# Kernel optimization log

Hardware: AMD Instinct MI355X
Metric: run time of the kernel (lower is better)

Reference implementation:

```python
import jax, jax.numpy as jnp
import numpy as np

N = 100000
E = 1600000
IN_DIM = 128
OUT_DIM = 128
H = 4
HD = OUT_DIM // H  # 32
NEG_SLOPE = 0.2
EPS_SOFTMAX = 1e-8
EPS_LN = 1e-5


def setup_inputs() -> dict:
    key = jax.random.key(0)
    ks = jax.random.split(key, 6)
    h = jax.random.normal(ks[0], (N, IN_DIM), dtype=jnp.float32)
    edge_index = jax.random.randint(ks[1], (2, E), 0, N, dtype=jnp.int32)
    W = jax.random.normal(ks[2], (IN_DIM, OUT_DIM), dtype=jnp.float32) / np.sqrt(IN_DIM)
    W_self = jax.random.normal(ks[3], (IN_DIM, OUT_DIM), dtype=jnp.float32) / np.sqrt(IN_DIM)
    a_in = jax.random.normal(ks[4], (H, 2 * HD), dtype=jnp.float32) * 0.01
    a_out = jax.random.normal(ks[5], (H, 2 * HD), dtype=jnp.float32) * 0.01
    bias = jnp.zeros((OUT_DIM,), dtype=jnp.float32)
    ln_gamma = jnp.ones((OUT_DIM,), dtype=jnp.float32)
    ln_beta = jnp.zeros((OUT_DIM,), dtype=jnp.float32)
    return {"h": h, "edge_index": edge_index, "W": W, "W_self": W_self,
            "a_in": a_in, "a_out": a_out, "bias": bias,
            "ln_gamma": ln_gamma, "ln_beta": ln_beta}


def _attention_aggregate(h_proj, sender, receiver, attn_vec, num_nodes):
    # h_proj: (N, H, HD); sender/receiver: (E,); attn_vec: (H, 2*HD)
    h_sender = h_proj[sender]      # (E, H, HD)
    h_receiver = h_proj[receiver]  # (E, H, HD)
    # e = sum over concat([h_sender, h_receiver]) * attn_vec, split halves
    e = (jnp.einsum('ehd,hd->eh', h_sender, attn_vec[:, :HD])
         + jnp.einsum('ehd,hd->eh', h_receiver, attn_vec[:, HD:]))
    e = jax.nn.leaky_relu(e, NEG_SLOPE)
    e_max = jax.ops.segment_max(e, receiver, num_segments=num_nodes)  # (N, H)
    alpha = jnp.exp(e - e_max[receiver])
    alpha_sum = jax.ops.segment_sum(alpha, receiver, num_segments=num_nodes)
    alpha = alpha / (alpha_sum[receiver] + EPS_SOFTMAX)
    msg = h_sender * alpha[..., None]  # (E, H, HD)
    return jax.ops.segment_sum(msg, receiver, num_segments=num_nodes)  # (N, H, HD)


def reference(h, edge_index, W, W_self, a_in, a_out, bias, ln_gamma, ln_beta):
    n = h.shape[0]
    h_proj = (h @ W).reshape(n, H, HD)
    h_self = h @ W_self
    src, dst = edge_index[0], edge_index[1]
    h_in = _attention_aggregate(h_proj, src, dst, a_in, n)   # 'in' direction
    h_out = _attention_aggregate(h_proj, dst, src, a_out, n)  # 'out' direction
    combined = h_self + h_in.reshape(n, -1) + h_out.reshape(n, -1) + bias
    mean = combined.mean(axis=-1, keepdims=True)
    var = combined.var(axis=-1, keepdims=True)
    normed = (combined - mean) * jax.lax.rsqrt(var + EPS_LN)
    return normed * ln_gamma + ln_beta
```

## Files before the change

kernel.cpp:

```cpp
#include <hip/hip_runtime.h>
#include <math.h>

#define HEADS 4
#define HD 32
#define DIM 128
#define NEG_SLOPE 0.2f
#define EPS_SM 1e-8f
#define EPS_LN 1e-5f
#define GROWS 64
#define SH1 9
#define PB 128

__device__ __forceinline__ float lrelu(float x) { return x > 0.f ? x : NEG_SLOPE * x; }
__device__ __forceinline__ unsigned bf16rne(float x) {
    unsigned b = __float_as_uint(x);
    return (b + 0x7fffu + ((b >> 16) & 1u)) >> 16;
}

template<int LIM> __device__ __forceinline__ void rmax4(float& a, float& b, float& c, float& d) {
#pragma unroll
    for (int s = 1; s < LIM; s <<= 1) {
        a = fmaxf(a, __shfl_xor(a, s, 64));
        b = fmaxf(b, __shfl_xor(b, s, 64));
        c = fmaxf(c, __shfl_xor(c, s, 64));
        d = fmaxf(d, __shfl_xor(d, s, 64));
    }
}
template<int LIM> __device__ __forceinline__ void rsum4(float& a, float& b, float& c, float& d) {
#pragma unroll
    for (int s = 1; s < LIM; s <<= 1) {
        a += __shfl_xor(a, s, 64);
        b += __shfl_xor(b, s, 64);
        c += __shfl_xor(c, s, 64);
        d += __shfl_xor(d, s, 64);
    }
}

__global__ __launch_bounds__(256) void dual_gemm_k(const float* __restrict__ h,
                                                   const float* __restrict__ W,
                                                   const float* __restrict__ V,
                                                   const float* __restrict__ a_in,
                                                   const float* __restrict__ a_out,
                                                   float* __restrict__ h_self,
                                                   unsigned* __restrict__ hp_pk,
                                                   float* __restrict__ pA0, float* __restrict__ pA1,
                                                   float* __restrict__ pB0, float* __restrict__ pB1,
                                                   int N) {
    __shared__ float As[32][GROWS];
    __shared__ float Ws[32][DIM];
    __shared__ float Vs[32][DIM];
    __shared__ float ainL[256], aoutL[256];
    const int tid = threadIdx.x;
    const int cg = tid & 15;
    const int rg = tid >> 4;
    const int row0 = blockIdx.x * GROWS;

    ainL[tid] = a_in[tid];
    aoutL[tid] = a_out[tid];

    float accP[4][8], accS[4][8];
#pragma unroll
    for (int r = 0; r < 4; ++r)
#pragma unroll
        for (int c = 0; c < 8; ++c) { accP[r][c] = 0.f; accS[r][c] = 0.f; }

    for (int kc = 0; kc < 4; ++kc) {
        __syncthreads();
#pragma unroll
        for (int p = 0; p < 2; ++p) {
            int f = tid + p * 256;
            int r = f >> 3, c4 = f & 7;
            float4 v = make_float4(0.f, 0.f, 0.f, 0.f);
            if (row0 + r < N) v = ((const float4*)h)[(size_t)(row0 + r) * 32 + kc * 8 + c4];
            As[c4 * 4 + 0][r] = v.x;
            As[c4 * 4 + 1][r] = v.y;
            As[c4 * 4 + 2][r] = v.z;
            As[c4 * 4 + 3][r] = v.w;
        }
#pragma unroll
        for (int p = 0; p < 4; ++p) {
            int f = tid + p * 256;
            int lk = f >> 5, c4 = f & 31;
            ((float4*)&Ws[lk][0])[c4] = ((const float4*)W)[(size_t)(kc * 32 + lk) * 32 + c4];
            ((float4*)&Vs[lk][0])[c4] = ((const float4*)V)[(size_t)(kc * 32 + lk) * 32 + c4];
        }
        __syncthreads();
#pragma unroll
        for (int kk = 0; kk < 32; ++kk) {
            float4 a = *(const float4*)&As[kk][rg * 4];
            float4 w0 = *(const float4*)&Ws[kk][cg * 8];
            float4 w1 = *(const float4*)&Ws[kk][cg * 8 + 4];
            float4 v0 = *(const float4*)&Vs[kk][cg * 8];
            float4 v1 = *(const float4*)&Vs[kk][cg * 8 + 4];
            float av[4] = {a.x, a.y, a.z, a.w};
            float wv[8] = {w0.x, w0.y, w0.z, w0.w, w1.x, w1.y, w1.z, w1.w};
            float vv[8] = {v0.x, v0.y, v0.z, v0.w, v1.x, v1.y, v1.z, v1.w};
#pragma unroll
            for (int r = 0; r < 4; ++r)
#pragma unroll
                for (int c = 0; c < 8; ++c) {
                    accP[r][c] += av[r] * wv[c];
                    accS[r][c] += av[r] * vv[c];
                }
        }
    }

#pragma unroll
    for (int r = 0; r < 4; ++r) {
        int row = row0 + rg * 4 + r;
        if (row < N) {
            float4 s0 = make_float4(accS[r][0], accS[r][1], accS[r][2], accS[r][3]);
            float4 s1 = make_float4(accS[r][4], accS[r][5], accS[r][6], accS[r][7]);
            ((float4*)h_self)[(size_t)row * 32 + cg * 2] = s0;
            ((float4*)h_self)[(size_t)row * 32 + cg * 2 + 1] = s1;
        }
    }

    const int head = cg >> 2, qi = cg & 3;
#pragma unroll
    for (int r = 0; r < 4; ++r) {
        float d0 = 0.f, d1 = 0.f, d2 = 0.f, d3 = 0.f;
#pragma unroll
        for (int c = 0; c < 8; ++c) {
            float v = accP[r][c];
            int k = head * 64 + qi * 8 + c;
            d0 += v * ainL[k];
            d1 += v * ainL[k + 32];
            d2 += v * aoutL[k];
            d3 += v * aoutL[k + 32];
        }
        d0 += __shfl_xor(d0, 1, 64); d0 += __shfl_xor(d0, 2, 64);
        d1 += __shfl_xor(d1, 1, 64); d1 += __shfl_xor(d1, 2, 64);
        d2 += __shfl_xor(d2, 1, 64); d2 += __shfl_xor(d2, 2, 64);
        d3 += __shfl_xor(d3, 1, 64); d3 += __shfl_xor(d3, 2, 64);
        if (qi == 0) {
            int row = row0 + rg * 4 + r;
            if (row < N) {
                pA0[row * 4 + head] = d0;
                pA1[row * 4 + head] = d1;
                pB0[row * 4 + head] = d2;
                pB1[row * 4 + head] = d3;
            }
        }
    }

    __syncthreads();
    float* lds2 = &Ws[0][0];
    if (cg >= 8) {
#pragma unroll
        for (int r = 0; r < 4; ++r) {
            int rl = rg * 4 + r;
#pragma unroll
            for (int c = 0; c < 8; ++c) lds2[rl * 64 + (cg - 8) * 8 + c] = accP[r][c];
        }
    }
    __syncthreads();
    if (cg < 8) {
#pragma unroll
        for (int r = 0; r < 4; ++r) {
            int rl = rg * 4 + r;
            int row = row0 + rl;
            if (row < N) {
                unsigned pks[8];
#pragma unroll
                for (int c = 0; c < 8; ++c)
                    pks[c] = bf16rne(accP[r][c]) | (bf16rne(lds2[rl * 64 + cg * 8 + c]) << 16);
                uint4* dst = (uint4*)(hp_pk + (size_t)row * 64 + cg * 8);
                dst[0] = make_uint4(pks[0], pks[1], pks[2], pks[3]);
                dst[1] = make_uint4(pks[4], pks[5], pks[6], pks[7]);
            }
        }
    }
}

__global__ __launch_bounds__(256) void part1a_k(const int* __restrict__ ei, int* __restrict__ cntmat,
                                                int E, int N, int NBIN) {
    __shared__ int lcnt[512];
    const int t = threadIdx.x;
    const int CH = (E + gridDim.x - 1) / gridDim.x;
    const int e0 = blockIdx.x * CH;
    const int e1 = min(e0 + CH, E);
    for (int i = t; i < 512; i += 256) lcnt[i] = 0;
    __syncthreads();
    for (int e = e0 + t; e < e1; e += 256) {
        int s = ei[e], d = ei[E + e];
        atomicAdd(&lcnt[d >> SH1], 1);
        atomicAdd(&lcnt[(N + s) >> SH1], 1);
    }
    __syncthreads();
    for (int i = t; i < NBIN; i += 256) cntmat[i * PB + blockIdx.x] = lcnt[i];
}

__global__ __launch_bounds__(128) void scanB_k(const int* __restrict__ cntmat,
                                               int* __restrict__ blkoff, int* __restrict__ btot) {
    __shared__ int ls[PB];
    const int bin = blockIdx.x;
    const int t = threadIdx.x;
    int v = cntmat[bin * PB + t];
    ls[t] = v;
    __syncthreads();
#pragma unroll
    for (int d = 1; d < PB; d <<= 1) {
        int u = (t >= d) ? ls[t - d] : 0;
        __syncthreads();
        ls[t] += u;
        __syncthreads();
    }
    blkoff[bin * PB + t] = ls[t] - v;
    if (t == PB - 1) btot[bin] = ls[t];
}

__global__ __launch_bounds__(256) void scanC_k(const int* __restrict__ btot,
                                               int* __restrict__ bbase, int NBIN, int twoE) {
    __shared__ int ls[256];
    int t = threadIdx.x;
    int i0 = 2 * t, i1 = 2 * t + 1;
    int v0 = (i0 < NBIN) ? btot[i0] : 0;
    int v1 = (i1 < NBIN) ? btot[i1] : 0;
    int pair = v0 + v1;
    ls[t] = pair;
    __syncthreads();
#pragma unroll
    for (int d = 1; d < 256; d <<= 1) {
        int u = (t >= d) ? ls[t - d] : 0;
        __syncthreads();
        ls[t] += u;
        __syncthreads();
    }
    int excl = ls[t] - pair;
    if (i0 < NBIN) bbase[i0] = excl;
    if (i1 < NBIN) bbase[i1] = excl + v0;
    if (t == 0) bbase[NBIN] = twoE;
}

__global__ __launch_bounds__(256) void part1b_k(const int* __restrict__ ei,
                                                const int* __restrict__ bbase,
                                                const int* __restrict__ blkoff,
                                                unsigned* __restrict__ rec, int E, int N, int NBIN) {
    __shared__ int gb[512];
    __shared__ int lcur[512];
    const int t = threadIdx.x;
    const int CH = (E + gridDim.x - 1) / gridDim.x;
    const int e0 = blockIdx.x * CH;
    const int e1 = min(e0 + CH, E);
    for (int i = t; i < 512; i += 256) lcur[i] = 0;
    for (int i = t; i < NBIN; i += 256) gb[i] = bbase[i] + blkoff[i * PB + blockIdx.x];
    __syncthreads();
    for (int e = e0 + t; e < e1; e += 256) {
        int s = ei[e], d = ei[E + e];
        int b1 = d >> SH1;
        int r1 = atomicAdd(&lcur[b1], 1);
        rec[gb[b1] + r1] = (unsigned)s | ((unsigned)(d & 511) << 20);
        int so = N + s;
        int b2 = so >> SH1;
        int r2 = atomicAdd(&lcur[b2], 1);
        rec[gb[b2] + r2] = (unsigned)d | ((unsigned)(so & 511) << 20);
    }
}

__global__ __launch_bounds__(256) void build2_k(const unsigned* __restrict__ rec,
                                                const int* __restrict__ bbase,
                                                int* __restrict__ off, int* __restrict__ csr,
                                                int M, int twoE, int NBIN) {
    __shared__ int lcnt[512];
    __shared__ int lcur[512];
    __shared__ int ls[256];
    const int b = blockIdx.x;
    const int t = threadIdx.x;
    const int base = bbase[b];
    const int cnt = bbase[b + 1] - base;
    const int seg0 = b << SH1;
    for (int i = t; i < 512; i += 256) lcnt[i] = 0;
    __syncthreads();
    for (int k = t; k < cnt; k += 256) atomicAdd(&lcnt[rec[base + k] >> 20], 1);
    __syncthreads();
    int v0 = lcnt[2 * t], v1 = lcnt[2 * t + 1];
    int pair = v0 + v1;
    ls[t] = pair;
    __syncthreads();
#pragma unroll
    for (int d = 1; d < 256; d <<= 1) {
        int u = (t >= d) ? ls[t - d] : 0;
        __syncthreads();
        ls[t] += u;
        __syncthreads();
    }
    int excl = ls[t] - pair;
    lcur[2 * t] = excl;
    lcur[2 * t + 1] = excl + v0;
    int sg = seg0 + 2 * t;
    if (sg < M) off[sg] = base + excl;
    if (sg + 1 < M) off[sg + 1] = base + excl + v0;
    if (b == NBIN - 1 && t == 0) off[M] = twoE;
    __syncthreads();
    for (int k = t; k < cnt; k += 256) {
        unsigned r = rec[base + k];
        int pos = atomicAdd(&lcur[r >> 20], 1);
        csr[base + pos] = (int)(r & 0xFFFFFu);
    }
}

__global__ __launch_bounds__(256) void node_aggr_ln_k(const unsigned* __restrict__ hp_pk,
                                                      const float* __restrict__ h_self,
                                                      const float* __restrict__ pA0, const float* __restrict__ pA1,
                                                      const float* __restrict__ pB0, const float* __restrict__ pB1,
                                                      const int* __restrict__ off, const int* __restrict__ csr,
                                                      const float* __restrict__ bias,
                                                      const float* __restrict__ gamma,
                                                      const float* __restrict__ beta,
                                                      float* __restrict__ out, int N) {
    __shared__ uint4 lw[4][64];
    const int wave = threadIdx.x >> 6;
    const int lane = threadIdx.x & 63;
    const int n = blockIdx.x * 4 + wave;
    if (n >= N) return;
    const int l15 = lane & 15;
    const int q = lane >> 4;
    const unsigned lwoff = (unsigned)((q << 4) + ((l15 >> 3) << 3));
    const char* lwbase = (const char*)&lw[wave][0];
    const uint4* __restrict__ hpp4 = (const uint4*)hp_pk;

    float alo0 = 0.f, alo1 = 0.f, alo2 = 0.f, alo3 = 0.f;
    float ahi0 = 0.f, ahi1 = 0.f, ahi2 = 0.f, ahi3 = 0.f;

#pragma unroll
    for (int dir = 0; dir < 2; ++dir) {
        const int seg = (dir == 0) ? n : N + n;
        const int beg = off[seg], end = off[seg + 1];
        const int len = end - beg;
        if (len == 0) continue;
        const float* __restrict__ p0 = (dir == 0) ? pA0 : pB0;
        const float* __restrict__ p1 = (dir == 0) ? pA1 : pB1;
        float4 r1 = ((const float4*)p1)[n];

        if (len <= 64) {
            int sid = 0;
            float e0 = -INFINITY, e1 = -INFINITY, e2 = -INFINITY, e3 = -INFINITY;
            if (lane < len) {
                sid = csr[beg + lane];
                float4 r0 = ((const float4*)p0)[sid];
                e0 = lrelu(r0.x + r1.x);
                e1 = lrelu(r0.y + r1.y);
                e2 = lrelu(r0.z + r1.z);
                e3 = lrelu(r0.w + r1.w);
            }
            float m0 = e0, m1 = e1, m2 = e2, m3 = e3;
            if (len <= 16)      rmax4<16>(m0, m1, m2, m3);
            else if (len <= 32) rmax4<32>(m0, m1, m2, m3);
            else                rmax4<64>(m0, m1, m2, m3);
            float w0 = 0.f, w1 = 0.f, w2 = 0.f, w3 = 0.f;
            if (lane < len) {
                w0 = expf(e0 - m0); w1 = expf(e1 - m1);
                w2 = expf(e2 - m2); w3 = expf(e3 - m3);
            }
            float s0 = w0, s1 = w1, s2 = w2, s3 = w3;
            if (len <= 16)      rsum4<16>(s0, s1, s2, s3);
            else if (len <= 32) rsum4<32>(s0, s1, s2, s3);
            else                rsum4<64>(s0, s1, s2, s3);
            w0 *= 1.f / (s0 + EPS_SM);
            w1 *= 1.f / (s1 + EPS_SM);
            w2 *= 1.f / (s2 + EPS_SM);
            w3 *= 1.f / (s3 + EPS_SM);
            unsigned pkA = bf16rne(w0) | (bf16rne(w2) << 16);
            unsigned pkB = bf16rne(w1) | (bf16rne(w3) << 16);
            lw[wave][lane] = make_uint4(pkA, (unsigned)sid, pkB, (unsigned)sid);
            const int nt = (len + 3) >> 2;
#pragma unroll 2
            for (int t = 0; t < nt; ++t) {
                uint2 wv = *(const uint2*)(lwbase + t * 64 + lwoff);
                uint4 v = hpp4[((size_t)wv.y << 4) + l15];
                float wa = __uint_as_float(wv.x << 16);
                float wb = __uint_as_float(wv.x & 0xffff0000u);
                alo0 += wa * __uint_as_float(v.x << 16);
                ahi0 += wb * __uint_as_float(v.x & 0xffff0000u);
                alo1 += wa * __uint_as_float(v.y << 16);
                ahi1 += wb * __uint_as_float(v.y & 0xffff0000u);
                alo2 += wa * __uint_as_float(v.z << 16);
                ahi2 += wb * __uint_as_float(v.z & 0xffff0000u);
                alo3 += wa * __uint_as_float(v.w << 16);
                ahi3 += wb * __uint_as_float(v.w & 0xffff0000u);
            }
        } else {
            float m0 = -INFINITY, m1 = -INFINITY, m2 = -INFINITY, m3 = -INFINITY;
            for (int base = beg; base < end; base += 64) {
                int j = base + lane;
                if (j < end) {
                    int sid = csr[j];
                    float4 r0 = ((const float4*)p0)[sid];
                    m0 = fmaxf(m0, lrelu(r0.x + r1.x));
                    m1 = fmaxf(m1, lrelu(r0.y + r1.y));
                    m2 = fmaxf(m2, lrelu(r0.z + r1.z));
                    m3 = fmaxf(m3, lrelu(r0.w + r1.w));
                }
            }
            rmax4<64>(m0, m1, m2, m3);
            float s0 = 0.f, s1 = 0.f, s2 = 0.f, s3 = 0.f;
            for (int base = beg; base < end; base += 64) {
                int j = base + lane;
                if (j < end) {
                    int sid = csr[j];
                    float4 r0 = ((const float4*)p0)[sid];
                    s0 += expf(lrelu(r0.x + r1.x) - m0);
                    s1 += expf(lrelu(r0.y + r1.y) - m1);
                    s2 += expf(lrelu(r0.z + r1.z) - m2);
                    s3 += expf(lrelu(r0.w + r1.w) - m3);
                }
            }
            rsum4<64>(s0, s1, s2, s3);
            const float is0 = 1.f / (s0 + EPS_SM);
            const float is1 = 1.f / (s1 + EPS_SM);
            const float is2 = 1.f / (s2 + EPS_SM);
            const float is3 = 1.f / (s3 + EPS_SM);
            for (int base = beg; base < end; base += 64) {
                int cnt = min(64, end - base);
                int sid = 0;
                float w0 = 0.f, w1 = 0.f, w2 = 0.f, w3 = 0.f;
                if (lane < cnt) {
                    sid = csr[base + lane];
                    float4 r0 = ((const float4*)p0)[sid];
                    w0 = expf(lrelu(r0.x + r1.x) - m0) * is0;
                    w1 = expf(lrelu(r0.y + r1.y) - m1) * is1;
                    w2 = expf(lrelu(r0.z + r1.z) - m2) * is2;
                    w3 = expf(lrelu(r0.w + r1.w) - m3) * is3;
                }
                unsigned pkA = bf16rne(w0) | (bf16rne(w2) << 16);
                unsigned pkB = bf16rne(w1) | (bf16rne(w3) << 16);
                lw[wave][lane] = make_uint4(pkA, (unsigned)sid, pkB, (unsigned)sid);
                const int nt = (cnt + 3) >> 2;
#pragma unroll 2
                for (int t = 0; t < nt; ++t) {
                    uint2 wv = *(const uint2*)(lwbase + t * 64 + lwoff);
                    uint4 v = hpp4[((size_t)wv.y << 4) + l15];
                    float wa = __uint_as_float(wv.x << 16);
                    float wb = __uint_as_float(wv.x & 0xffff0000u);
                    alo0 += wa * __uint_as_float(v.x << 16);
                    ahi0 += wb * __uint_as_float(v.x & 0xffff0000u);
                    alo1 += wa * __uint_as_float(v.y << 16);
                    ahi1 += wb * __uint_as_float(v.y & 0xffff0000u);
                    alo2 += wa * __uint_as_float(v.z << 16);
                    ahi2 += wb * __uint_as_float(v.z & 0xffff0000u);
                    alo3 += wa * __uint_as_float(v.w << 16);
                    ahi3 += wb * __uint_as_float(v.w & 0xffff0000u);
                }
            }
        }
    }

#pragma unroll
    for (int s = 16; s < 64; s <<= 1) {
        alo0 += __shfl_xor(alo0, s, 64); alo1 += __shfl_xor(alo1, s, 64);
        alo2 += __shfl_xor(alo2, s, 64); alo3 += __shfl_xor(alo3, s, 64);
        ahi0 += __shfl_xor(ahi0, s, 64); ahi1 += __shfl_xor(ahi1, s, 64);
        ahi2 += __shfl_xor(ahi2, s, 64); ahi3 += __shfl_xor(ahi3, s, 64);
    }

    size_t bb = (size_t)n * DIM;
    float4 hs0 = *(const float4*)(h_self + bb + 4 * l15);
    float4 hs1 = *(const float4*)(h_self + bb + 64 + 4 * l15);
    float4 b0 = *(const float4*)(bias + 4 * l15);
    float4 b1 = *(const float4*)(bias + 64 + 4 * l15);
    float x0 = hs0.x + alo0 + b0.x;
    float x1 = hs0.y + alo1 + b0.y;
    float x2 = hs0.z + alo2 + b0.z;
    float x3 = hs0.w + alo3 + b0.w;
    float y0 = hs1.x + ahi0 + b1.x;
    float y1 = hs1.y + ahi1 + b1.y;
    float y2 = hs1.z + ahi2 + b1.z;
    float y3 = hs1.w + ahi3 + b1.w;
    float sum = x0 + x1 + x2 + x3 + y0 + y1 + y2 + y3;
    float sq = x0 * x0 + x1 * x1 + x2 * x2 + x3 * x3
             + y0 * y0 + y1 * y1 + y2 * y2 + y3 * y3;
#pragma unroll
    for (int m = 1; m < 64; m <<= 1) {
        sum += __shfl_xor(sum, m, 64);
        sq += __shfl_xor(sq, m, 64);
    }
    float mean = sum * (1.f / 512.f);
    float var = sq * (1.f / 512.f) - mean * mean;
    float inv = rsqrtf(var + EPS_LN);
    if (lane < 16) {
        float4 g0 = *(const float4*)(gamma + 4 * l15);
        float4 g1 = *(const float4*)(gamma + 64 + 4 * l15);
        float4 be0 = *(const float4*)(beta + 4 * l15);
        float4 be1 = *(const float4*)(beta + 64 + 4 * l15);
        float4 o0 = make_float4((x0 - mean) * inv * g0.x + be0.x,
                                (x1 - mean) * inv * g0.y + be0.y,
                                (x2 - mean) * inv * g0.z + be0.z,
                                (x3 - mean) * inv * g0.w + be0.w);
        float4 o1 = make_float4((y0 - mean) * inv * g1.x + be1.x,
                                (y1 - mean) * inv * g1.y + be1.y,
                                (y2 - mean) * inv * g1.z + be1.z,
                                (y3 - mean) * inv * g1.w + be1.w);
        *(float4*)(out + bb + 4 * l15) = o0;
        *(float4*)(out + bb + 64 + 4 * l15) = o1;
    }
}

extern "C" void kernel_launch(void* const* d_in, const int* in_sizes, int n_in,
                              void* d_out, int out_size, void* d_ws, size_t ws_size,
                              hipStream_t stream) {
    const float* h      = (const float*)d_in[0];
    const int*   ei     = (const int*)d_in[1];
    const float* W      = (const float*)d_in[2];
    const float* W_self = (const float*)d_in[3];
    const float* a_in   = (const float*)d_in[4];
    const float* a_out  = (const float*)d_in[5];
    const float* bias   = (const float*)d_in[6];
    const float* gamma  = (const float*)d_in[7];
    const float* beta   = (const float*)d_in[8];
    float* out = (float*)d_out;

    const int N = in_sizes[0] / DIM;
    const int E = in_sizes[1] / 2;
    const int M = 2 * N;
    const int NBIN = (M + (1 << SH1) - 1) >> SH1;
    const int twoE = 2 * E;

    float* ws = (float*)d_ws;
    size_t off_f = 0;
    float* h_self = ws + off_f; off_f += (size_t)N * DIM;
    unsigned* hp_pk = (unsigned*)(ws + off_f); off_f += (size_t)N * 64;
    float* pA0 = ws + off_f; off_f += (size_t)N * 4;
    float* pA1 = ws + off_f; off_f += (size_t)N * 4;
    float* pB0 = ws + off_f; off_f += (size_t)N * 4;
    float* pB1 = ws + off_f; off_f += (size_t)N * 4;
    int* ip = (int*)(ws + off_f);
    size_t off_i = 0;
    int* cntmat = ip + off_i; off_i += (size_t)NBIN * PB;
    int* blkoff = ip + off_i; off_i += (size_t)NBIN * PB;
    int* btot   = ip + off_i; off_i += NBIN;
    int* bbase  = ip + off_i; off_i += (size_t)NBIN + 1;
    int* off    = ip + off_i; off_i += (size_t)M + 1;
    unsigned* rec = (unsigned*)(ip + off_i); off_i += (size_t)twoE;
    int* csr    = ip + off_i; off_i += (size_t)twoE;

    part1a_k<<<PB, 256, 0, stream>>>(ei, cntmat, E, N, NBIN);
    scanB_k<<<NBIN, PB, 0, stream>>>(cntmat, blkoff, btot);
    scanC_k<<<1, 256, 0, stream>>>(btot, bbase, NBIN, twoE);
    part1b_k<<<PB, 256, 0, stream>>>(ei, bbase, blkoff, rec, E, N, NBIN);
    build2_k<<<NBIN, 256, 0, stream>>>(rec, bbase, off, csr, M, twoE, NBIN);

    dual_gemm_k<<<(N + GROWS - 1) / GROWS, 256, 0, stream>>>(h, W, W_self, a_in, a_out,
                                                             h_self, hp_pk, pA0, pA1, pB0, pB1, N);

    node_aggr_ln_k<<<(N + 3) / 4, 256, 0, stream>>>(hp_pk, h_self, pA0, pA1, pB0, pB1,
                                                    off, csr, bias, gamma, beta, out, N);
}
```

Measured before the change: 454.3 us.

## Drop softmax max pass, use fast exp, packed FMA, and prefetch GEMM tiles

Removes the segment-max computation from the edge softmax and exponentiates logits directly with __expf, eliminating a full gather pass for long segments and the max shuffles for short ones. The accumulation is restructured as float2 FMAs to encourage packed FMA instructions. The dual GEMM now prefetches the next K chunk into registers while computing the current one. Skipping max-subtraction risks overflow if logits were large, and it adds register pressure in the GEMM.

```diff
diff --git a/kernel.cpp b/kernel.cpp
--- a/kernel.cpp
+++ b/kernel.cpp
@@ -16,16 +16,10 @@
     unsigned b = __float_as_uint(x);
     return (b + 0x7fffu + ((b >> 16) & 1u)) >> 16;
 }
-
-template<int LIM> __device__ __forceinline__ void rmax4(float& a, float& b, float& c, float& d) {
-#pragma unroll
-    for (int s = 1; s < LIM; s <<= 1) {
-        a = fmaxf(a, __shfl_xor(a, s, 64));
-        b = fmaxf(b, __shfl_xor(b, s, 64));
-        c = fmaxf(c, __shfl_xor(c, s, 64));
-        d = fmaxf(d, __shfl_xor(d, s, 64));
-    }
-}
+__device__ __forceinline__ float2 pkfma(float2 v, float2 w, float2 c) {
+    return make_float2(fmaf(v.x, w.x, c.x), fmaf(v.y, w.y, c.y));
+}
+
 template<int LIM> __device__ __forceinline__ void rsum4(float& a, float& b, float& c, float& d) {
 #pragma unroll
     for (int s = 1; s < LIM; s <<= 1) {
@@ -64,27 +58,45 @@
 #pragma unroll
         for (int c = 0; c < 8; ++c) { accP[r][c] = 0.f; accS[r][c] = 0.f; }
 
-    for (int kc = 0; kc < 4; ++kc) {
-        __syncthreads();
+    float4 pha[2], pw[4], pv[4];
+    auto load_chunk = [&](int kc) {
 #pragma unroll
         for (int p = 0; p < 2; ++p) {
             int f = tid + p * 256;
             int r = f >> 3, c4 = f & 7;
             float4 v = make_float4(0.f, 0.f, 0.f, 0.f);
             if (row0 + r < N) v = ((const float4*)h)[(size_t)(row0 + r) * 32 + kc * 8 + c4];
-            As[c4 * 4 + 0][r] = v.x;
-            As[c4 * 4 + 1][r] = v.y;
-            As[c4 * 4 + 2][r] = v.z;
-            As[c4 * 4 + 3][r] = v.w;
+            pha[p] = v;
         }
 #pragma unroll
         for (int p = 0; p < 4; ++p) {
             int f = tid + p * 256;
             int lk = f >> 5, c4 = f & 31;
-            ((float4*)&Ws[lk][0])[c4] = ((const float4*)W)[(size_t)(kc * 32 + lk) * 32 + c4];
-            ((float4*)&Vs[lk][0])[c4] = ((const float4*)V)[(size_t)(kc * 32 + lk) * 32 + c4];
-        }
-        __syncthreads();
+            pw[p] = ((const float4*)W)[(size_t)(kc * 32 + lk) * 32 + c4];
+            pv[p] = ((const float4*)V)[(size_t)(kc * 32 + lk) * 32 + c4];
+        }
+    };
+
+    load_chunk(0);
+    for (int kc = 0; kc < 4; ++kc) {
+#pragma unroll
+        for (int p = 0; p < 2; ++p) {
+            int f = tid + p * 256;
+            int r = f >> 3, c4 = f & 7;
+            As[c4 * 4 + 0][r] = pha[p].x;
+            As[c4 * 4 + 1][r] = pha[p].y;
+            As[c4 * 4 + 2][r] = pha[p].z;
+            As[c4 * 4 + 3][r] = pha[p].w;
+        }
+#pragma unroll
+        for (int p = 0; p < 4; ++p) {
+            int f = tid + p * 256;
+            int lk = f >> 5, c4 = f & 31;
+            ((float4*)&Ws[lk][0])[c4] = pw[p];
+            ((float4*)&Vs[lk][0])[c4] = pv[p];
+        }
+        __syncthreads();
+        if (kc < 3) load_chunk(kc + 1);
 #pragma unroll
         for (int kk = 0; kk < 32; ++kk) {
             float4 a = *(const float4*)&As[kk][rg * 4];
@@ -103,6 +115,7 @@
                     accS[r][c] += av[r] * vv[c];
                 }
         }
+        __syncthreads();
     }
 
 #pragma unroll
@@ -320,8 +333,8 @@
     const char* lwbase = (const char*)&lw[wave][0];
     const uint4* __restrict__ hpp4 = (const uint4*)hp_pk;
 
-    float alo0 = 0.f, alo1 = 0.f, alo2 = 0.f, alo3 = 0.f;
-    float ahi0 = 0.f, ahi1 = 0.f, ahi2 = 0.f, ahi3 = 0.f;
+    float2 a0 = make_float2(0.f, 0.f), a1 = make_float2(0.f, 0.f);
+    float2 a2 = make_float2(0.f, 0.f), a3 = make_float2(0.f, 0.f);
 
 #pragma unroll
     for (int dir = 0; dir < 2; ++dir) {
@@ -335,23 +348,14 @@
 
         if (len <= 64) {
             int sid = 0;
-            float e0 = -INFINITY, e1 = -INFINITY, e2 = -INFINITY, e3 = -INFINITY;
+            float w0 = 0.f, w1 = 0.f, w2 = 0.f, w3 = 0.f;
             if (lane < len) {
                 sid = csr[beg + lane];
                 float4 r0 = ((const float4*)p0)[sid];
-                e0 = lrelu(r0.x + r1.x);
-                e1 = lrelu(r0.y + r1.y);
-                e2 = lrelu(r0.z + r1.z);
-                e3 = lrelu(r0.w + r1.w);
-            }
-            float m0 = e0, m1 = e1, m2 = e2, m3 = e3;
-            if (len <= 16)      rmax4<16>(m0, m1, m2, m3);
-            else if (len <= 32) rmax4<32>(m0, m1, m2, m3);
-            else                rmax4<64>(m0, m1, m2, m3);
-            float w0 = 0.f, w1 = 0.f, w2 = 0.f, w3 = 0.f;
-            if (lane < len) {
-                w0 = expf(e0 - m0); w1 = expf(e1 - m1);
-                w2 = expf(e2 - m2); w3 = expf(e3 - m3);
+                w0 = __expf(lrelu(r0.x + r1.x));
+                w1 = __expf(lrelu(r0.y + r1.y));
+                w2 = __expf(lrelu(r0.z + r1.z));
+                w3 = __expf(lrelu(r0.w + r1.w));
             }
             float s0 = w0, s1 = w1, s2 = w2, s3 = w3;
             if (len <= 16)      rsum4<16>(s0, s1, s2, s3);
@@ -369,41 +373,24 @@
             for (int t = 0; t < nt; ++t) {
                 uint2 wv = *(const uint2*)(lwbase + t * 64 + lwoff);
                 uint4 v = hpp4[((size_t)wv.y << 4) + l15];
-                float wa = __uint_as_float(wv.x << 16);
-                float wb = __uint_as_float(wv.x & 0xffff0000u);
-                alo0 += wa * __uint_as_float(v.x << 16);
-                ahi0 += wb * __uint_as_float(v.x & 0xffff0000u);
-                alo1 += wa * __uint_as_float(v.y << 16);
-                ahi1 += wb * __uint_as_float(v.y & 0xffff0000u);
-                alo2 += wa * __uint_as_float(v.z << 16);
-                ahi2 += wb * __uint_as_float(v.z & 0xffff0000u);
-                alo3 += wa * __uint_as_float(v.w << 16);
-                ahi3 += wb * __uint_as_float(v.w & 0xffff0000u);
+                float2 w = make_float2(__uint_as_float(wv.x << 16),
+                                       __uint_as_float(wv.x & 0xffff0000u));
+                a0 = pkfma(make_float2(__uint_as_float(v.x << 16), __uint_as_float(v.x & 0xffff0000u)), w, a0);
+                a1 = pkfma(make_float2(__uint_as_float(v.y << 16), __uint_as_float(v.y & 0xffff0000u)), w, a1);
+                a2 = pkfma(make_float2(__uint_as_float(v.z << 16), __uint_as_float(v.z & 0xffff0000u)), w, a2);
+                a3 = pkfma(make_float2(__uint_as_float(v.w << 16), __uint_as_float(v.w & 0xffff0000u)), w, a3);
             }
         } else {
-            float m0 = -INFINITY, m1 = -INFINITY, m2 = -INFINITY, m3 = -INFINITY;
-            for (int base = beg; base < end; base += 64) {
-                int j = base + lane;
-                if (j < end) {
-                    int sid = csr[j];
-                    float4 r0 = ((const float4*)p0)[sid];
-                    m0 = fmaxf(m0, lrelu(r0.x + r1.x));
-                    m1 = fmaxf(m1, lrelu(r0.y + r1.y));
-                    m2 = fmaxf(m2, lrelu(r0.z + r1.z));
-                    m3 = fmaxf(m3, lrelu(r0.w + r1.w));
-                }
-            }
-            rmax4<64>(m0, m1, m2, m3);
             float s0 = 0.f, s1 = 0.f, s2 = 0.f, s3 = 0.f;
             for (int base = beg; base < end; base += 64) {
                 int j = base + lane;
                 if (j < end) {
                     int sid = csr[j];
                     float4 r0 = ((const float4*)p0)[sid];
-                    s0 += expf(lrelu(r0.x + r1.x) - m0);
-                    s1 += expf(lrelu(r0.y + r1.y) - m1);
-                    s2 += expf(lrelu(r0.z + r1.z) - m2);
-                    s3 += expf(lrelu(r0.w + r1.w) - m3);
+                    s0 += __expf(lrelu(r0.x + r1.x));
+                    s1 += __expf(lrelu(r0.y + r1.y));
+                    s2 += __expf(lrelu(r0.z + r1.z));
+                    s3 += __expf(lrelu(r0.w + r1.w));
                 }
             }
             rsum4<64>(s0, s1, s2, s3);
@@ -418,10 +405,10 @@
                 if (lane < cnt) {
                     sid = csr[base + lane];
                     float4 r0 = ((const float4*)p0)[sid];
-                    w0 = expf(lrelu(r0.x + r1.x) - m0) * is0;
-                    w1 = expf(lrelu(r0.y + r1.y) - m1) * is1;
-                    w2 = expf(lrelu(r0.z + r1.z) - m2) * is2;
-                    w3 = expf(lrelu(r0.w + r1.w) - m3) * is3;
+                    w0 = __expf(lrelu(r0.x + r1.x)) * is0;
+                    w1 = __expf(lrelu(r0.y + r1.y)) * is1;
+                    w2 = __expf(lrelu(r0.z + r1.z)) * is2;
+                    w3 = __expf(lrelu(r0.w + r1.w)) * is3;
                 }
                 unsigned pkA = bf16rne(w0) | (bf16rne(w2) << 16);
                 unsigned pkB = bf16rne(w1) | (bf16rne(w3) << 16);
@@ -431,16 +418,12 @@
                 for (int t = 0; t < nt; ++t) {
                     uint2 wv = *(const uint2*)(lwbase + t * 64 + lwoff);
                     uint4 v = hpp4[((size_t)wv.y << 4) + l15];
-                    float wa = __uint_as_float(wv.x << 16);
-                    float wb = __uint_as_float(wv.x & 0xffff0000u);
-                    alo0 += wa * __uint_as_float(v.x << 16);
-                    ahi0 += wb * __uint_as_float(v.x & 0xffff0000u);
-                    alo1 += wa * __uint_as_float(v.y << 16);
-                    ahi1 += wb * __uint_as_float(v.y & 0xffff0000u);
-                    alo2 += wa * __uint_as_float(v.z << 16);
-                    ahi2 += wb * __uint_as_float(v.z & 0xffff0000u);
-                    alo3 += wa * __uint_as_float(v.w << 16);
-                    ahi3 += wb * __uint_as_float(v.w & 0xffff0000u);
+                    float2 w = make_float2(__uint_as_float(wv.x << 16),
+                                           __uint_as_float(wv.x & 0xffff0000u));
+                    a0 = pkfma(make_float2(__uint_as_float(v.x << 16), __uint_as_float(v.x & 0xffff0000u)), w, a0);
+                    a1 = pkfma(make_float2(__uint_as_float(v.y << 16), __uint_as_float(v.y & 0xffff0000u)), w, a1);
+                    a2 = pkfma(make_float2(__uint_as_float(v.z << 16), __uint_as_float(v.z & 0xffff0000u)), w, a2);
+                    a3 = pkfma(make_float2(__uint_as_float(v.w << 16), __uint_as_float(v.w & 0xffff0000u)), w, a3);
                 }
             }
         }
@@ -448,10 +431,10 @@
 
 #pragma unroll
     for (int s = 16; s < 64; s <<= 1) {
-        alo0 += __shfl_xor(alo0, s, 64); alo1 += __shfl_xor(alo1, s, 64);
-        alo2 += __shfl_xor(alo2, s, 64); alo3 += __shfl_xor(alo3, s, 64);
-        ahi0 += __shfl_xor(ahi0, s, 64); ahi1 += __shfl_xor(ahi1, s, 64);
-        ahi2 += __shfl_xor(ahi2, s, 64); ahi3 += __shfl_xor(ahi3, s, 64);
+        a0.x += __shfl_xor(a0.x, s, 64); a0.y += __shfl_xor(a0.y, s, 64);
+        a1.x += __shfl_xor(a1.x, s, 64); a1.y += __shfl_xor(a1.y, s, 64);
+        a2.x += __shfl_xor(a2.x, s, 64); a2.y += __shfl_xor(a2.y, s, 64);
+        a3.x += __shfl_xor(a3.x, s, 64); a3.y += __shfl_xor(a3.y, s, 64);
     }
 
     size_t bb = (size_t)n * DIM;
@@ -459,14 +442,14 @@
     float4 hs1 = *(const float4*)(h_self + bb + 64 + 4 * l15);
     float4 b0 = *(const float4*)(bias + 4 * l15);
     float4 b1 = *(const float4*)(bias + 64 + 4 * l15);
-    float x0 = hs0.x + alo0 + b0.x;
-    float x1 = hs0.y + alo1 + b0.y;
-    float x2 = hs0.z + alo2 + b0.z;
-    float x3 = hs0.w + alo3 + b0.w;
-    float y0 = hs1.x + ahi0 + b1.x;
-    float y1 = hs1.y + ahi1 + b1.y;
-    float y2 = hs1.z + ahi2 + b1.z;
-    float y3 = hs1.w + ahi3 + b1.w;
+    float x0 = hs0.x + a0.x + b0.x;
+    float x1 = hs0.y + a1.x + b0.y;
+    float x2 = hs0.z + a2.x + b0.z;
+    float x3 = hs0.w + a3.x + b0.w;
+    float y0 = hs1.x + a0.y + b1.x;
+    float y1 = hs1.y + a1.y + b1.y;
+    float y2 = hs1.z + a2.y + b1.z;
+    float y3 = hs1.w + a3.y + b1.w;
     float sum = x0 + x1 + x2 + x3 + y0 + y1 + y2 + y3;
     float sq = x0 * x0 + x1 * x1 + x2 * x2 + x3 * x3
              + y0 * y0 + y1 * y1 + y2 * y2 + y3 * y3;
```

After: 475.2 us. 4.6% more time.
